# Performance work log

Measured on AMD Instinct MI355X. Metric: run time of the kernel, lower is better.

The kernel has to match this reference:

```python
import jax, jax.numpy as jnp
import numpy as np

B = 4096
D_IN = 1024
HIDDEN = [1024, 512, 256]
NUM_DOMAINS = 8


def _glorot(key, shape):
    fan_in, fan_out = shape[-2], shape[-1]
    std = np.sqrt(2.0 / (fan_in + fan_out)).astype(np.float32)
    return jax.random.normal(key, shape, dtype=jnp.float32) * std


def setup_inputs() -> dict:
    key = jax.random.key(0)
    keys = jax.random.split(key, 16)
    dims = [D_IN] + HIDDEN  # per-layer (in, out) = (dims[i], dims[i+1])
    inp = {
        "x": jax.random.normal(keys[0], (B, D_IN), dtype=jnp.float32),
        "indicator": jax.random.randint(keys[1], (B,), 0, NUM_DOMAINS, dtype=jnp.int32),
    }
    for i in range(len(HIDDEN)):
        inp[f"sk{i}"] = _glorot(keys[2 + i], (dims[i], dims[i + 1]))
        inp[f"sb{i}"] = jnp.zeros((dims[i + 1],), dtype=jnp.float32)
        # per-domain kernels stacked on leading domain axis: (D, in, out)
        inp[f"dk{i}"] = _glorot(keys[6 + i], (NUM_DOMAINS, dims[i], dims[i + 1]))
        inp[f"db{i}"] = jnp.zeros((NUM_DOMAINS, dims[i + 1]), dtype=jnp.float32)
    return inp


def reference(x, indicator, sk0, sb0, dk0, db0, sk1, sb1, dk1, db1, sk2, sb2, dk2, db2):
    shared_k = [sk0, sk1, sk2]
    shared_b = [sb0, sb1, sb2]
    domain_k = [dk0, dk1, dk2]
    domain_b = [db0, db1, db2]
    D = dk0.shape[0]
    # Replicate input across all domains: [B, D, d_in] (source computes every domain stack)
    h = jnp.broadcast_to(x[:, None, :], (x.shape[0], D, x.shape[1]))
    for sk, sb, dk, db in zip(shared_k, shared_b, domain_k, domain_b):
        w_eff = sk[None, :, :] * dk          # [D, in, out]  fused shared*domain weights
        b_eff = sb[None, :] + db             # [D, out]
        h = jnp.einsum('bdi,dio->bdo', h, w_eff) + b_eff[None, :, :]
        h = jax.nn.relu(h)                   # all layers use 'relu' (no output_activation)
    one_hot = jax.nn.one_hot(indicator, D, dtype=h.dtype)  # [B, D]
    return jnp.einsum('bdo,bd->bo', h, one_hot)
```

## Files before the change

### kernel.cpp

```cpp
#include <hip/hip_runtime.h>

#define NROWS 4096
#define NDOM 8

typedef short short8 __attribute__((ext_vector_type(8)));
typedef float floatx4 __attribute__((ext_vector_type(4)));
typedef unsigned short ushort8v __attribute__((ext_vector_type(8)));

__device__ __forceinline__ unsigned short f2bf(float f) {
    union { float f; unsigned u; } v; v.f = f;
    unsigned r = v.u + 0x7FFFu + ((v.u >> 16) & 1u);
    return (unsigned short)(r >> 16);
}

__device__ __forceinline__ void dma16(const void* g, void* l) {
    __builtin_amdgcn_global_load_lds(
        (const __attribute__((address_space(1))) unsigned*)g,
        (__attribute__((address_space(3))) unsigned*)l, 16, 0, 0);
}

template <int N>
__device__ __forceinline__ void wait_vmcnt() {
    static_assert(N == 0 || N == 2 || N == 3 || N == 4 || N == 6 || N == 8, "unsupported vmcnt");
    if constexpr (N == 0) asm volatile("s_waitcnt vmcnt(0)" ::: "memory");
    else if constexpr (N == 2) asm volatile("s_waitcnt vmcnt(2)" ::: "memory");
    else if constexpr (N == 3) asm volatile("s_waitcnt vmcnt(3)" ::: "memory");
    else if constexpr (N == 4) asm volatile("s_waitcnt vmcnt(4)" ::: "memory");
    else if constexpr (N == 6) asm volatile("s_waitcnt vmcnt(6)" ::: "memory");
    else if constexpr (N == 8) asm volatile("s_waitcnt vmcnt(8)" ::: "memory");
}


template <int K, int N>
__device__ __forceinline__ void weff_tile(const float* __restrict__ sk,
                                          const float* __restrict__ dk,
                                          unsigned short* __restrict__ wt,
                                          unsigned short* __restrict__ lds,
                                          int local) {
    const int d = local & 7;
    const int rest = local >> 3;
    const int k0 = (rest & (K / 256 - 1)) * 256;
    const int n0 = (rest / (K / 256)) * 64;
    const int t = threadIdx.x;

    const int n = t & 63;
    const int kg = (t >> 6) * 64;
#pragma unroll
    for (int c8 = 0; c8 < 8; ++c8) {
        const int kb = k0 + kg + c8 * 8;
        unsigned short wb[8];
#pragma unroll
        for (int i = 0; i < 8; ++i) {
            int k = kb + i;
            wb[i] = f2bf(sk[(size_t)k * N + n0 + n] * dk[((size_t)d * K + k) * N + n0 + n]);
        }
        int ch = (kg + c8 * 8) >> 3;
        int phys = ch ^ (n & 31);
        *(ushort8v*)&lds[n * 256 + phys * 8] = *(ushort8v*)wb;
    }
    __syncthreads();

#pragma unroll
    for (int it = 0; it < 4; ++it) {
        const int nn = (t >> 4) + it * 16;
        const int c = t & 15;
        ushort8v a = *(ushort8v*)&lds[nn * 256 + ((2 * c) ^ (nn & 31)) * 8];
        ushort8v b = *(ushort8v*)&lds[nn * 256 + ((2 * c + 1) ^ (nn & 31)) * 8];
        unsigned short* dst = wt + ((size_t)d * N + n0 + nn) * K + k0 + c * 16;
        *(ushort8v*)dst = a;
        *(ushort8v*)(dst + 8) = b;
    }
}

__global__ void precompute_kernel(const float* __restrict__ x,
                                  const int* __restrict__ ind,
                                  const float* __restrict__ sk0, const float* __restrict__ dk0,
                                  const float* __restrict__ sk1, const float* __restrict__ dk1,
                                  const float* __restrict__ sk2, const float* __restrict__ dk2,
                                  unsigned short* __restrict__ xb,
                                  unsigned short* __restrict__ w0t,
                                  unsigned short* __restrict__ w1t,
                                  unsigned short* __restrict__ w2t,
                                  int* __restrict__ offsets,
                                  int* __restrict__ rowidx) {
    __shared__ union SMem {
        unsigned short wtile[64 * 256];
        struct {
            unsigned short cnt[256][NDOM];
            int base[256][NDOM];
            int dom_total[NDOM];
            int dom_off[NDOM + 1];
        } sort;
    } smem;

    const int b = blockIdx.x;
    const int t = threadIdx.x;

    if (b < 256) {
#pragma unroll
        for (int pass = 0; pass < 8; ++pass) {
            int row = b * 16 + pass * 2 + (t >> 7);
            int ch = t & 127;
            const float* src = x + (size_t)row * 1024 + ch * 8;
            floatx4 v0 = *(const floatx4*)src;
            floatx4 v1 = *(const floatx4*)(src + 4);
            unsigned short o[8];
            o[0] = f2bf(v0[0]); o[1] = f2bf(v0[1]); o[2] = f2bf(v0[2]); o[3] = f2bf(v0[3]);
            o[4] = f2bf(v1[0]); o[5] = f2bf(v1[1]); o[6] = f2bf(v1[2]); o[7] = f2bf(v1[3]);
            *(ushort8v*)(xb + (size_t)row * 1024 + ch * 8) = *(ushort8v*)o;
        }
    } else if (b < 256 + 512) {
        weff_tile<1024, 1024>(sk0, dk0, w0t, smem.wtile, b - 256);
    } else if (b < 256 + 512 + 256) {
        weff_tile<1024, 512>(sk1, dk1, w1t, smem.wtile, b - (256 + 512));
    } else if (b < 256 + 512 + 256 + 64) {
        weff_tile<512, 256>(sk2, dk2, w2t, smem.wtile, b - (256 + 512 + 256));
    } else {
        int myind[16];
#pragma unroll
        for (int i = 0; i < 16; ++i) myind[i] = ind[t * 16 + i];
        unsigned short c[NDOM];
#pragma unroll
        for (int d = 0; d < NDOM; ++d) c[d] = 0;
#pragma unroll
        for (int i = 0; i < 16; ++i) c[myind[i]]++;
#pragma unroll
        for (int d = 0; d < NDOM; ++d) smem.sort.cnt[t][d] = c[d];
        __syncthreads();
        if (t < NDOM) {
            int acc = 0;
            for (int ch = 0; ch < 256; ++ch) { smem.sort.base[ch][t] = acc; acc += smem.sort.cnt[ch][t]; }
            smem.sort.dom_total[t] = acc;
        }
        __syncthreads();
        if (t == 0) {
            int acc = 0;
            for (int d = 0; d < NDOM; ++d) { smem.sort.dom_off[d] = acc; acc += smem.sort.dom_total[d]; }
            smem.sort.dom_off[NDOM] = acc;
        }
        __syncthreads();
        int pos[NDOM];
#pragma unroll
        for (int d = 0; d < NDOM; ++d) pos[d] = smem.sort.dom_off[d] + smem.sort.base[t][d];
#pragma unroll
        for (int i = 0; i < 16; ++i) {
            int dm = myind[i];
            rowidx[pos[dm]++] = t * 16 + i;
        }
        if (t <= NDOM) offsets[t] = smem.sort.dom_off[t];
    }
}

template <int FM, int FN, int MSLOTS, int K, int N, bool GATHER, bool SCATTER>
__launch_bounds__(256)
__global__ void star_gemm(const unsigned short* __restrict__ Ab,
                          const unsigned short* __restrict__ Wt,
                          const float* __restrict__ sb,
                          const float* __restrict__ db,
                          float* __restrict__ OutF,
                          unsigned short* __restrict__ OutB,
                          const int* __restrict__ offsets,
                          const int* __restrict__ rowidx) {
    constexpr int BM = 32 * FM;
    constexpr int BN = 32 * FN;
    constexpr int NK = K / 64;
    constexpr int AI = BM / 32;
    constexpr int WI = BN / 32;
    constexpr int CNT = AI + WI;

    __shared__ __align__(128) unsigned short As[2][BM * 64];
    __shared__ __align__(128) unsigned short Ws[2][BN * 64];

    const int gid = blockIdx.x;
    const int d = gid & 7;
    const int mslot = (gid >> 3) % MSLOTS;
    const int n0 = (gid / (8 * MSLOTS)) * BN;

    const int bstart = offsets[d];
    const int bend = offsets[d + 1];
    const int bsize = bend - bstart;

    const int tid = threadIdx.x;
    const int lane = tid & 63;
    const int w = tid >> 6;
    const int wy = w >> 1;
    const int wx = w & 1;
    const int lm = lane & 15;
    const int quad = lane >> 4;

    const int lrow = lane >> 3;
    const int phys = lane & 7;

    float bias[FN];
#pragma unroll
    for (int j = 0; j < FN; ++j) {
        int n = n0 + wx * FN * 16 + j * 16 + lm;
        bias[j] = sb[n] + db[d * N + n];
    }

    const unsigned short* wsrc[WI];
#pragma unroll
    for (int j = 0; j < WI; ++j) {
        int nr0 = (w * WI + j) * 8;
        int nn = nr0 + lrow;
        int ch = phys ^ (nn & 7);
        wsrc[j] = Wt + ((size_t)d * N + n0 + nn) * K + ch * 8;
    }

    for (int mt = mslot; mt * BM < bsize; mt += MSLOTS) {
        const int row_start = bstart + mt * BM;

        const unsigned short* asrc[AI];
#pragma unroll
        for (int j = 0; j < AI; ++j) {
            int m0 = (w * AI + j) * 8;
            int mm = m0 + lrow;
            int ch = phys ^ (mm & 7);
            int p = row_start + mm; if (p >= bend) p = bend - 1;
            int src = GATHER ? rowidx[p] : p;
            asrc[j] = Ab + (size_t)src * K + ch * 8;
        }

        auto dma_tiles = [&](int kt, int buf) {
            const int k0 = kt * 64;
#pragma unroll
            for (int j = 0; j < AI; ++j)
                dma16(asrc[j] + k0, &As[buf][(w * AI + j) * 512]);
#pragma unroll
            for (int j = 0; j < WI; ++j)
                dma16(wsrc[j] + k0, &Ws[buf][(w * WI + j) * 512]);
        };

        dma_tiles(0, 0);

        floatx4 acc[FM][FN];
#pragma unroll
        for (int i = 0; i < FM; ++i)
#pragma unroll
            for (int j = 0; j < FN; ++j) acc[i][j] = floatx4{0.f, 0.f, 0.f, 0.f};

#pragma unroll 2
        for (int kt = 0; kt < NK; ++kt) {
            const int buf = kt & 1;
            if (kt + 1 < NK) {
                dma_tiles(kt + 1, 1 - buf);
                wait_vmcnt<CNT>();
            } else {
                wait_vmcnt<0>();
            }
            __builtin_amdgcn_s_barrier();
            asm volatile("" ::: "memory");

            short8 av[2][FM], wv[2][FN];
#pragma unroll
            for (int kk = 0; kk < 2; ++kk) {
#pragma unroll
                for (int i = 0; i < FM; ++i) {
                    int m = wy * FM * 16 + i * 16 + lm;
                    int pc = (kk * 4 + quad) ^ (m & 7);
                    av[kk][i] = *(const short8*)&As[buf][m * 64 + pc * 8];
                }
#pragma unroll
                for (int j = 0; j < FN; ++j) {
                    int n = wx * FN * 16 + j * 16 + lm;
                    int pc = (kk * 4 + quad) ^ (n & 7);
                    wv[kk][j] = *(const short8*)&Ws[buf][n * 64 + pc * 8];
                }
            }
            asm volatile("s_waitcnt lgkmcnt(0)" ::: "memory");
            __builtin_amdgcn_sched_barrier(0);
            __builtin_amdgcn_s_barrier();
            asm volatile("" ::: "memory");

            __builtin_amdgcn_s_setprio(1);
#pragma unroll
            for (int kk = 0; kk < 2; ++kk)
#pragma unroll
                for (int i = 0; i < FM; ++i)
#pragma unroll
                    for (int j = 0; j < FN; ++j)
                        acc[i][j] = __builtin_amdgcn_mfma_f32_16x16x32_bf16(
                            av[kk][i], wv[kk][j], acc[i][j], 0, 0, 0);
            __builtin_amdgcn_s_setprio(0);
        }

#pragma unroll
        for (int i = 0; i < FM; ++i) {
#pragma unroll
            for (int rg = 0; rg < 4; ++rg) {
                int m = wy * FM * 16 + i * 16 + quad * 4 + rg;
                int p = row_start + m;
                if (p < bend) {
                    if constexpr (SCATTER) {
                        int orow = rowidx[p];
#pragma unroll
                        for (int j = 0; j < FN; ++j) {
                            int n = n0 + wx * FN * 16 + j * 16 + lm;
                            float v = acc[i][j][rg] + bias[j];
                            OutF[(size_t)orow * N + n] = v > 0.f ? v : 0.f;
                        }
                    } else {
#pragma unroll
                        for (int j = 0; j < FN; ++j) {
                            int n = n0 + wx * FN * 16 + j * 16 + lm;
                            float v = acc[i][j][rg] + bias[j];
                            OutB[(size_t)p * N + n] = f2bf(v > 0.f ? v : 0.f);
                        }
                    }
                }
            }
        }
    }
}

extern "C" void kernel_launch(void* const* d_in, const int* in_sizes, int n_in,
                              void* d_out, int out_size, void* d_ws, size_t ws_size,
                              hipStream_t stream) {
    const float* x = (const float*)d_in[0];
    const int* ind = (const int*)d_in[1];
    const float* sk0 = (const float*)d_in[2];
    const float* sb0 = (const float*)d_in[3];
    const float* dk0 = (const float*)d_in[4];
    const float* db0 = (const float*)d_in[5];
    const float* sk1 = (const float*)d_in[6];
    const float* sb1 = (const float*)d_in[7];
    const float* dk1 = (const float*)d_in[8];
    const float* db1 = (const float*)d_in[9];
    const float* sk2 = (const float*)d_in[10];
    const float* sb2 = (const float*)d_in[11];
    const float* dk2 = (const float*)d_in[12];
    const float* db2 = (const float*)d_in[13];
    float* out = (float*)d_out;

    char* ws = (char*)d_ws;
    int* offsets = (int*)ws;
    int* rowidx = (int*)(ws + 256);
    unsigned short* xb  = (unsigned short*)(ws + 32768);
    unsigned short* h1  = xb + (size_t)NROWS * 1024;
    unsigned short* h2  = h1 + (size_t)NROWS * 1024;
    unsigned short* w0t = h2 + (size_t)NROWS * 512;
    unsigned short* w1t = w0t + (size_t)NDOM * 1024 * 1024;
    unsigned short* w2t = w1t + (size_t)NDOM * 512 * 1024;

    precompute_kernel<<<256 + 512 + 256 + 64 + 1, 256, 0, stream>>>(
        x, ind, sk0, dk0, sk1, dk1, sk2, dk2, xb, w0t, w1t, w2t, offsets, rowidx);

    star_gemm<2, 2, 8, 1024, 1024, true, false><<<1024, 256, 0, stream>>>(
        xb, w0t, sb0, db0, nullptr, h1, offsets, rowidx);
    star_gemm<2, 2, 8, 1024, 512, false, false><<<512, 256, 0, stream>>>(
        h1, w1t, sb1, db1, nullptr, h2, offsets, rowidx);
    star_gemm<1, 2, 16, 512, 256, false, true><<<512, 256, 0, stream>>>(
        h2, w2t, sb2, db2, out, nullptr, offsets, rowidx);
}
```

Baseline: 191.2 us.

## Overlap layer-1/2 weight prep with layer-0 GEMM in a fused launch

Moves the fused weight computation for layers 1 and 2 out of the precompute kernel and into extra blocks of the layer-0 GEMM launch, so that weight preparation runs concurrently with the first GEMM instead of before it. The GEMM body is factored into a device function that takes shared-memory pointers, and layer 0 switches to a wider N tile (FN=4) with half as many GEMM blocks. This shortens the critical path of the precompute stage. In exchange the layer-0 GEMM blocks share the GPU with weight-prep blocks, and the wider tile changes occupancy and register use.

New measurement: 192.8 us. About the same (+0.8%).

```diff
diff --git a/kernel.cpp b/kernel.cpp
--- a/kernel.cpp
+++ b/kernel.cpp
@@ -29,7 +29,6 @@
     else if constexpr (N == 6) asm volatile("s_waitcnt vmcnt(6)" ::: "memory");
     else if constexpr (N == 8) asm volatile("s_waitcnt vmcnt(8)" ::: "memory");
 }
-
 
 template <int K, int N>
 __device__ __forceinline__ void weff_tile(const float* __restrict__ sk,
@@ -75,12 +74,8 @@
 __global__ void precompute_kernel(const float* __restrict__ x,
                                   const int* __restrict__ ind,
                                   const float* __restrict__ sk0, const float* __restrict__ dk0,
-                                  const float* __restrict__ sk1, const float* __restrict__ dk1,
-                                  const float* __restrict__ sk2, const float* __restrict__ dk2,
                                   unsigned short* __restrict__ xb,
                                   unsigned short* __restrict__ w0t,
-                                  unsigned short* __restrict__ w1t,
-                                  unsigned short* __restrict__ w2t,
                                   int* __restrict__ offsets,
                                   int* __restrict__ rowidx) {
     __shared__ union SMem {
@@ -111,10 +106,6 @@
         }
     } else if (b < 256 + 512) {
         weff_tile<1024, 1024>(sk0, dk0, w0t, smem.wtile, b - 256);
-    } else if (b < 256 + 512 + 256) {
-        weff_tile<1024, 512>(sk1, dk1, w1t, smem.wtile, b - (256 + 512));
-    } else if (b < 256 + 512 + 256 + 64) {
-        weff_tile<512, 256>(sk2, dk2, w2t, smem.wtile, b - (256 + 512 + 256));
     } else {
         int myind[16];
 #pragma unroll
@@ -148,6 +139,169 @@
             rowidx[pos[dm]++] = t * 16 + i;
         }
         if (t <= NDOM) offsets[t] = smem.sort.dom_off[t];
+    }
+}
+
+template <int FM, int FN, int MSLOTS, int K, int N, bool GATHER, bool SCATTER>
+__device__ __forceinline__ void star_gemm_body(
+        unsigned short* __restrict__ As,
+        unsigned short* __restrict__ Ws,
+        const unsigned short* __restrict__ Ab,
+        const unsigned short* __restrict__ Wt,
+        const float* __restrict__ sb,
+        const float* __restrict__ db,
+        float* __restrict__ OutF,
+        unsigned short* __restrict__ OutB,
+        const int* __restrict__ offsets,
+        const int* __restrict__ rowidx,
+        int gid) {
+    constexpr int BM = 32 * FM;
+    constexpr int BN = 32 * FN;
+    constexpr int NK = K / 64;
+    constexpr int AI = BM / 32;
+    constexpr int WI = BN / 32;
+    constexpr int CNT = AI + WI;
+    constexpr int ASZ = BM * 64;
+    constexpr int WSZ = BN * 64;
+
+    const int d = gid & 7;
+    const int mslot = (gid >> 3) % MSLOTS;
+    const int n0 = (gid / (8 * MSLOTS)) * BN;
+
+    const int bstart = offsets[d];
+    const int bend = offsets[d + 1];
+    const int bsize = bend - bstart;
+
+    const int tid = threadIdx.x;
+    const int lane = tid & 63;
+    const int w = tid >> 6;
+    const int wy = w >> 1;
+    const int wx = w & 1;
+    const int lm = lane & 15;
+    const int quad = lane >> 4;
+
+    const int lrow = lane >> 3;
+    const int phys = lane & 7;
+
+    float bias[FN];
+#pragma unroll
+    for (int j = 0; j < FN; ++j) {
+        int n = n0 + wx * FN * 16 + j * 16 + lm;
+        bias[j] = sb[n] + db[d * N + n];
+    }
+
+    const unsigned short* wsrc[WI];
+#pragma unroll
+    for (int j = 0; j < WI; ++j) {
+        int nr0 = (w * WI + j) * 8;
+        int nn = nr0 + lrow;
+        int ch = phys ^ (nn & 7);
+        wsrc[j] = Wt + ((size_t)d * N + n0 + nn) * K + ch * 8;
+    }
+
+    for (int mt = mslot; mt * BM < bsize; mt += MSLOTS) {
+        const int row_start = bstart + mt * BM;
+
+        const unsigned short* asrc[AI];
+#pragma unroll
+        for (int j = 0; j < AI; ++j) {
+            int m0 = (w * AI + j) * 8;
+            int mm = m0 + lrow;
+            int ch = phys ^ (mm & 7);
+            int p = row_start + mm; if (p >= bend) p = bend - 1;
+            int src = GATHER ? rowidx[p] : p;
+            asrc[j] = Ab + (size_t)src * K + ch * 8;
+        }
+
+        auto dma_tiles = [&](int kt, int buf) {
+            const int k0 = kt * 64;
+#pragma unroll
+            for (int j = 0; j < AI; ++j)
+                dma16(asrc[j] + k0, &As[buf * ASZ + (w * AI + j) * 512]);
+#pragma unroll
+            for (int j = 0; j < WI; ++j)
+                dma16(wsrc[j] + k0, &Ws[buf * WSZ + (w * WI + j) * 512]);
+        };
+
+        dma_tiles(0, 0);
+
+        floatx4 acc[FM][FN];
+#pragma unroll
+        for (int i = 0; i < FM; ++i)
+#pragma unroll
+            for (int j = 0; j < FN; ++j) acc[i][j] = floatx4{0.f, 0.f, 0.f, 0.f};
+
+#pragma unroll 2
+        for (int kt = 0; kt < NK; ++kt) {
+            const int buf = kt & 1;
+            if (kt + 1 < NK) {
+                dma_tiles(kt + 1, 1 - buf);
+                wait_vmcnt<CNT>();
+            } else {
+                wait_vmcnt<0>();
+            }
+            __builtin_amdgcn_s_barrier();
+            asm volatile("" ::: "memory");
+
+            short8 av[2][FM], wv[2][FN];
+#pragma unroll
+            for (int kk = 0; kk < 2; ++kk) {
+#pragma unroll
+                for (int i = 0; i < FM; ++i) {
+                    int m = wy * FM * 16 + i * 16 + lm;
+                    int pc = (kk * 4 + quad) ^ (m & 7);
+                    av[kk][i] = *(const short8*)&As[buf * ASZ + m * 64 + pc * 8];
+                }
+#pragma unroll
+                for (int j = 0; j < FN; ++j) {
+                    int n = wx * FN * 16 + j * 16 + lm;
+                    int pc = (kk * 4 + quad) ^ (n & 7);
+                    wv[kk][j] = *(const short8*)&Ws[buf * WSZ + n * 64 + pc * 8];
+                }
+            }
+            asm volatile("s_waitcnt lgkmcnt(0)" ::: "memory");
+            __builtin_amdgcn_sched_barrier(0);
+            __builtin_amdgcn_s_barrier();
+            asm volatile("" ::: "memory");
+
+            __builtin_amdgcn_s_setprio(1);
+#pragma unroll
+            for (int kk = 0; kk < 2; ++kk)
+#pragma unroll
+                for (int i = 0; i < FM; ++i)
+#pragma unroll
+                    for (int j = 0; j < FN; ++j)
+                        acc[i][j] = __builtin_amdgcn_mfma_f32_16x16x32_bf16(
+                            av[kk][i], wv[kk][j], acc[i][j], 0, 0, 0);
+            __builtin_amdgcn_s_setprio(0);
+        }
+
+#pragma unroll
+        for (int i = 0; i < FM; ++i) {
+#pragma unroll
+            for (int rg = 0; rg < 4; ++rg) {
+                int m = wy * FM * 16 + i * 16 + quad * 4 + rg;
+                int p = row_start + m;
+                if (p < bend) {
+                    if constexpr (SCATTER) {
+                        int orow = rowidx[p];
+#pragma unroll
+                        for (int j = 0; j < FN; ++j) {
+                            int n = n0 + wx * FN * 16 + j * 16 + lm;
+                            float v = acc[i][j][rg] + bias[j];
+                            OutF[(size_t)orow * N + n] = v > 0.f ? v : 0.f;
+                        }
+                    } else {
+#pragma unroll
+                        for (int j = 0; j < FN; ++j) {
+                            int n = n0 + wx * FN * 16 + j * 16 + lm;
+                            float v = acc[i][j][rg] + bias[j];
+                            OutB[(size_t)p * N + n] = f2bf(v > 0.f ? v : 0.f);
+                        }
+                    }
+                }
+            }
+        }
     }
 }
 
@@ -163,153 +317,32 @@
                           const int* __restrict__ rowidx) {
     constexpr int BM = 32 * FM;
     constexpr int BN = 32 * FN;
-    constexpr int NK = K / 64;
-    constexpr int AI = BM / 32;
-    constexpr int WI = BN / 32;
-    constexpr int CNT = AI + WI;
-
-    __shared__ __align__(128) unsigned short As[2][BM * 64];
-    __shared__ __align__(128) unsigned short Ws[2][BN * 64];
-
+    __shared__ __align__(128) unsigned short As[2 * BM * 64];
+    __shared__ __align__(128) unsigned short Ws[2 * BN * 64];
+    star_gemm_body<FM, FN, MSLOTS, K, N, GATHER, SCATTER>(
+        As, Ws, Ab, Wt, sb, db, OutF, OutB, offsets, rowidx, blockIdx.x);
+}
+
+__launch_bounds__(256)
+__global__ void l0_fused(const unsigned short* __restrict__ xb,
+                         const unsigned short* __restrict__ w0t,
+                         const float* __restrict__ sb0, const float* __restrict__ db0,
+                         unsigned short* __restrict__ h1,
+                         const float* __restrict__ sk1, const float* __restrict__ dk1,
+                         unsigned short* __restrict__ w1t,
+                         const float* __restrict__ sk2, const float* __restrict__ dk2,
+                         unsigned short* __restrict__ w2t,
+                         const int* __restrict__ offsets,
+                         const int* __restrict__ rowidx) {
+    __shared__ __align__(128) unsigned short smem[24576];
     const int gid = blockIdx.x;
-    const int d = gid & 7;
-    const int mslot = (gid >> 3) % MSLOTS;
-    const int n0 = (gid / (8 * MSLOTS)) * BN;
-
-    const int bstart = offsets[d];
-    const int bend = offsets[d + 1];
-    const int bsize = bend - bstart;
-
-    const int tid = threadIdx.x;
-    const int lane = tid & 63;
-    const int w = tid >> 6;
-    const int wy = w >> 1;
-    const int wx = w & 1;
-    const int lm = lane & 15;
-    const int quad = lane >> 4;
-
-    const int lrow = lane >> 3;
-    const int phys = lane & 7;
-
-    float bias[FN];
-#pragma unroll
-    for (int j = 0; j < FN; ++j) {
-        int n = n0 + wx * FN * 16 + j * 16 + lm;
-        bias[j] = sb[n] + db[d * N + n];
-    }
-
-    const unsigned short* wsrc[WI];
-#pragma unroll
-    for (int j = 0; j < WI; ++j) {
-        int nr0 = (w * WI + j) * 8;
-        int nn = nr0 + lrow;
-        int ch = phys ^ (nn & 7);
-        wsrc[j] = Wt + ((size_t)d * N + n0 + nn) * K + ch * 8;
-    }
-
-    for (int mt = mslot; mt * BM < bsize; mt += MSLOTS) {
-        const int row_start = bstart + mt * BM;
-
-        const unsigned short* asrc[AI];
-#pragma unroll
-        for (int j = 0; j < AI; ++j) {
-            int m0 = (w * AI + j) * 8;
-            int mm = m0 + lrow;
-            int ch = phys ^ (mm & 7);
-            int p = row_start + mm; if (p >= bend) p = bend - 1;
-            int src = GATHER ? rowidx[p] : p;
-            asrc[j] = Ab + (size_t)src * K + ch * 8;
-        }
-
-        auto dma_tiles = [&](int kt, int buf) {
-            const int k0 = kt * 64;
-#pragma unroll
-            for (int j = 0; j < AI; ++j)
-                dma16(asrc[j] + k0, &As[buf][(w * AI + j) * 512]);
-#pragma unroll
-            for (int j = 0; j < WI; ++j)
-                dma16(wsrc[j] + k0, &Ws[buf][(w * WI + j) * 512]);
-        };
-
-        dma_tiles(0, 0);
-
-        floatx4 acc[FM][FN];
-#pragma unroll
-        for (int i = 0; i < FM; ++i)
-#pragma unroll
-            for (int j = 0; j < FN; ++j) acc[i][j] = floatx4{0.f, 0.f, 0.f, 0.f};
-
-#pragma unroll 2
-        for (int kt = 0; kt < NK; ++kt) {
-            const int buf = kt & 1;
-            if (kt + 1 < NK) {
-                dma_tiles(kt + 1, 1 - buf);
-                wait_vmcnt<CNT>();
-            } else {
-                wait_vmcnt<0>();
-            }
-            __builtin_amdgcn_s_barrier();
-            asm volatile("" ::: "memory");
-
-            short8 av[2][FM], wv[2][FN];
-#pragma unroll
-            for (int kk = 0; kk < 2; ++kk) {
-#pragma unroll
-                for (int i = 0; i < FM; ++i) {
-                    int m = wy * FM * 16 + i * 16 + lm;
-                    int pc = (kk * 4 + quad) ^ (m & 7);
-                    av[kk][i] = *(const short8*)&As[buf][m * 64 + pc * 8];
-                }
-#pragma unroll
-                for (int j = 0; j < FN; ++j) {
-                    int n = wx * FN * 16 + j * 16 + lm;
-                    int pc = (kk * 4 + quad) ^ (n & 7);
-                    wv[kk][j] = *(const short8*)&Ws[buf][n * 64 + pc * 8];
-                }
-            }
-            asm volatile("s_waitcnt lgkmcnt(0)" ::: "memory");
-            __builtin_amdgcn_sched_barrier(0);
-            __builtin_amdgcn_s_barrier();
-            asm volatile("" ::: "memory");
-
-            __builtin_amdgcn_s_setprio(1);
-#pragma unroll
-            for (int kk = 0; kk < 2; ++kk)
-#pragma unroll
-                for (int i = 0; i < FM; ++i)
-#pragma unroll
-                    for (int j = 0; j < FN; ++j)
-                        acc[i][j] = __builtin_amdgcn_mfma_f32_16x16x32_bf16(
-                            av[kk][i], wv[kk][j], acc[i][j], 0, 0, 0);
-            __builtin_amdgcn_s_setprio(0);
-        }
-
-#pragma unroll
-        for (int i = 0; i < FM; ++i) {
-#pragma unroll
-            for (int rg = 0; rg < 4; ++rg) {
-                int m = wy * FM * 16 + i * 16 + quad * 4 + rg;
-                int p = row_start + m;
-                if (p < bend) {
-                    if constexpr (SCATTER) {
-                        int orow = rowidx[p];
-#pragma unroll
-                        for (int j = 0; j < FN; ++j) {
-                            int n = n0 + wx * FN * 16 + j * 16 + lm;
-                            float v = acc[i][j][rg] + bias[j];
-                            OutF[(size_t)orow * N + n] = v > 0.f ? v : 0.f;
-                        }
-                    } else {
-#pragma unroll
-                        for (int j = 0; j < FN; ++j) {
-                            int n = n0 + wx * FN * 16 + j * 16 + lm;
-                            float v = acc[i][j][rg] + bias[j];
-                            OutB[(size_t)p * N + n] = f2bf(v > 0.f ? v : 0.f);
-                        }
-                    }
-                }
-            }
-        }
+    if (gid < 512) {
+        star_gemm_body<2, 4, 8, 1024, 1024, true, false>(
+            smem, smem + 8192, xb, w0t, sb0, db0, nullptr, h1, offsets, rowidx, gid);
+    } else if (gid < 512 + 256) {
+        weff_tile<1024, 512>(sk1, dk1, w1t, smem, gid - 512);
+    } else {
+        weff_tile<512, 256>(sk2, dk2, w2t, smem, gid - (512 + 256));
     }
 }
 
@@ -342,11 +375,12 @@
     unsigned short* w1t = w0t + (size_t)NDOM * 1024 * 1024;
     unsigned short* w2t = w1t + (size_t)NDOM * 512 * 1024;
 
-    precompute_kernel<<<256 + 512 + 256 + 64 + 1, 256, 0, stream>>>(
-        x, ind, sk0, dk0, sk1, dk1, sk2, dk2, xb, w0t, w1t, w2t, offsets, rowidx);
-
-    star_gemm<2, 2, 8, 1024, 1024, true, false><<<1024, 256, 0, stream>>>(
-        xb, w0t, sb0, db0, nullptr, h1, offsets, rowidx);
+    precompute_kernel<<<256 + 512 + 1, 256, 0, stream>>>(
+        x, ind, sk0, dk0, xb, w0t, offsets, rowidx);
+
+    l0_fused<<<512 + 256 + 64, 256, 0, stream>>>(
+        xb, w0t, sb0, db0, h1, sk1, dk1, w1t, sk2, dk2, w2t, offsets, rowidx);
+
     star_gemm<2, 2, 8, 1024, 512, false, false><<<512, 256, 0, stream>>>(
         h1, w1t, sb1, db1, nullptr, h2, offsets, rowidx);
     star_gemm<1, 2, 16, 512, 256, false, true><<<512, 256, 0, stream>>>(
```

## Fuse precompute and three GEMM layers into one cooperative persistent kernel

Applied to the files above, without the earlier changes.

Replaces four separate launches with a single cooperative kernel of 256 blocks × 512 threads that loops over precompute work items and then runs each GEMM layer, separated by grid-wide syncs. GEMM tiles are reshaped for 8 waves (2×4) with larger BN, and MSLOTS for layer 0 drops to 4, which changes the per-block work distribution. It aims to remove launch gaps and tail effects between stages, at the cost of grid.sync overhead and only one 512-thread block per CU, which limits occupancy and latency hiding.

After: 470.5 us. +146.1%, slower.

```diff
diff --git a/kernel.cpp b/kernel.cpp
--- a/kernel.cpp
+++ b/kernel.cpp
@@ -1,4 +1,7 @@
 #include <hip/hip_runtime.h>
+#include <hip/hip_cooperative_groups.h>
+
+namespace cg = cooperative_groups;
 
 #define NROWS 4096
 #define NDOM 8
@@ -21,15 +24,12 @@
 
 template <int N>
 __device__ __forceinline__ void wait_vmcnt() {
-    static_assert(N == 0 || N == 2 || N == 3 || N == 4 || N == 6 || N == 8, "unsupported vmcnt");
+    static_assert(N == 0 || N == 2 || N == 3 || N == 4, "unsupported vmcnt");
     if constexpr (N == 0) asm volatile("s_waitcnt vmcnt(0)" ::: "memory");
     else if constexpr (N == 2) asm volatile("s_waitcnt vmcnt(2)" ::: "memory");
     else if constexpr (N == 3) asm volatile("s_waitcnt vmcnt(3)" ::: "memory");
     else if constexpr (N == 4) asm volatile("s_waitcnt vmcnt(4)" ::: "memory");
-    else if constexpr (N == 6) asm volatile("s_waitcnt vmcnt(6)" ::: "memory");
-    else if constexpr (N == 8) asm volatile("s_waitcnt vmcnt(8)" ::: "memory");
-}
-
+}
 
 template <int K, int N>
 __device__ __forceinline__ void weff_tile(const float* __restrict__ sk,
@@ -44,9 +44,9 @@
     const int t = threadIdx.x;
 
     const int n = t & 63;
-    const int kg = (t >> 6) * 64;
-#pragma unroll
-    for (int c8 = 0; c8 < 8; ++c8) {
+    const int kg = (t >> 6) * 32;
+#pragma unroll
+    for (int c8 = 0; c8 < 4; ++c8) {
         const int kb = k0 + kg + c8 * 8;
         unsigned short wb[8];
 #pragma unroll
@@ -61,8 +61,8 @@
     __syncthreads();
 
 #pragma unroll
-    for (int it = 0; it < 4; ++it) {
-        const int nn = (t >> 4) + it * 16;
+    for (int it = 0; it < 2; ++it) {
+        const int nn = (t >> 4) + it * 32;
         const int c = t & 15;
         ushort8v a = *(ushort8v*)&lds[nn * 256 + ((2 * c) ^ (nn & 31)) * 8];
         ushort8v b = *(ushort8v*)&lds[nn * 256 + ((2 * c + 1) ^ (nn & 31)) * 8];
@@ -72,51 +72,37 @@
     }
 }
 
-__global__ void precompute_kernel(const float* __restrict__ x,
-                                  const int* __restrict__ ind,
-                                  const float* __restrict__ sk0, const float* __restrict__ dk0,
-                                  const float* __restrict__ sk1, const float* __restrict__ dk1,
-                                  const float* __restrict__ sk2, const float* __restrict__ dk2,
-                                  unsigned short* __restrict__ xb,
-                                  unsigned short* __restrict__ w0t,
-                                  unsigned short* __restrict__ w1t,
-                                  unsigned short* __restrict__ w2t,
-                                  int* __restrict__ offsets,
-                                  int* __restrict__ rowidx) {
-    __shared__ union SMem {
-        unsigned short wtile[64 * 256];
-        struct {
-            unsigned short cnt[256][NDOM];
-            int base[256][NDOM];
-            int dom_total[NDOM];
-            int dom_off[NDOM + 1];
-        } sort;
-    } smem;
-
-    const int b = blockIdx.x;
+__device__ __forceinline__ void xb_task(const float* __restrict__ x,
+                                        unsigned short* __restrict__ xb, int b) {
     const int t = threadIdx.x;
-
-    if (b < 256) {
-#pragma unroll
-        for (int pass = 0; pass < 8; ++pass) {
-            int row = b * 16 + pass * 2 + (t >> 7);
-            int ch = t & 127;
-            const float* src = x + (size_t)row * 1024 + ch * 8;
-            floatx4 v0 = *(const floatx4*)src;
-            floatx4 v1 = *(const floatx4*)(src + 4);
-            unsigned short o[8];
-            o[0] = f2bf(v0[0]); o[1] = f2bf(v0[1]); o[2] = f2bf(v0[2]); o[3] = f2bf(v0[3]);
-            o[4] = f2bf(v1[0]); o[5] = f2bf(v1[1]); o[6] = f2bf(v1[2]); o[7] = f2bf(v1[3]);
-            *(ushort8v*)(xb + (size_t)row * 1024 + ch * 8) = *(ushort8v*)o;
-        }
-    } else if (b < 256 + 512) {
-        weff_tile<1024, 1024>(sk0, dk0, w0t, smem.wtile, b - 256);
-    } else if (b < 256 + 512 + 256) {
-        weff_tile<1024, 512>(sk1, dk1, w1t, smem.wtile, b - (256 + 512));
-    } else if (b < 256 + 512 + 256 + 64) {
-        weff_tile<512, 256>(sk2, dk2, w2t, smem.wtile, b - (256 + 512 + 256));
-    } else {
-        int myind[16];
+#pragma unroll
+    for (int pass = 0; pass < 4; ++pass) {
+        int row = b * 16 + pass * 4 + (t >> 7);
+        int ch = t & 127;
+        const float* src = x + (size_t)row * 1024 + ch * 8;
+        floatx4 v0 = *(const floatx4*)src;
+        floatx4 v1 = *(const floatx4*)(src + 4);
+        unsigned short o[8];
+        o[0] = f2bf(v0[0]); o[1] = f2bf(v0[1]); o[2] = f2bf(v0[2]); o[3] = f2bf(v0[3]);
+        o[4] = f2bf(v1[0]); o[5] = f2bf(v1[1]); o[6] = f2bf(v1[2]); o[7] = f2bf(v1[3]);
+        *(ushort8v*)(xb + (size_t)row * 1024 + ch * 8) = *(ushort8v*)o;
+    }
+}
+
+struct SortMem {
+    unsigned short cnt[256][NDOM];
+    int base[256][NDOM];
+    int dom_total[NDOM];
+    int dom_off[NDOM + 1];
+};
+
+__device__ __forceinline__ void sort_task(const int* __restrict__ ind,
+                                          int* __restrict__ offsets,
+                                          int* __restrict__ rowidx,
+                                          SortMem& s) {
+    const int t = threadIdx.x;
+    int myind[16];
+    if (t < 256) {
 #pragma unroll
         for (int i = 0; i < 16; ++i) myind[i] = ind[t * 16 + i];
         unsigned short c[NDOM];
@@ -125,53 +111,61 @@
 #pragma unroll
         for (int i = 0; i < 16; ++i) c[myind[i]]++;
 #pragma unroll
-        for (int d = 0; d < NDOM; ++d) smem.sort.cnt[t][d] = c[d];
-        __syncthreads();
-        if (t < NDOM) {
-            int acc = 0;
-            for (int ch = 0; ch < 256; ++ch) { smem.sort.base[ch][t] = acc; acc += smem.sort.cnt[ch][t]; }
-            smem.sort.dom_total[t] = acc;
-        }
-        __syncthreads();
-        if (t == 0) {
-            int acc = 0;
-            for (int d = 0; d < NDOM; ++d) { smem.sort.dom_off[d] = acc; acc += smem.sort.dom_total[d]; }
-            smem.sort.dom_off[NDOM] = acc;
-        }
-        __syncthreads();
+        for (int d = 0; d < NDOM; ++d) s.cnt[t][d] = c[d];
+    }
+    __syncthreads();
+    if (t < NDOM) {
+        int acc = 0;
+        for (int ch = 0; ch < 256; ++ch) { s.base[ch][t] = acc; acc += s.cnt[ch][t]; }
+        s.dom_total[t] = acc;
+    }
+    __syncthreads();
+    if (t == 0) {
+        int acc = 0;
+        for (int d = 0; d < NDOM; ++d) { s.dom_off[d] = acc; acc += s.dom_total[d]; }
+        s.dom_off[NDOM] = acc;
+    }
+    __syncthreads();
+    if (t < 256) {
         int pos[NDOM];
 #pragma unroll
-        for (int d = 0; d < NDOM; ++d) pos[d] = smem.sort.dom_off[d] + smem.sort.base[t][d];
+        for (int d = 0; d < NDOM; ++d) pos[d] = s.dom_off[d] + s.base[t][d];
 #pragma unroll
         for (int i = 0; i < 16; ++i) {
             int dm = myind[i];
             rowidx[pos[dm]++] = t * 16 + i;
         }
-        if (t <= NDOM) offsets[t] = smem.sort.dom_off[t];
+        if (t <= NDOM) offsets[t] = s.dom_off[t];
     }
 }
 
 template <int FM, int FN, int MSLOTS, int K, int N, bool GATHER, bool SCATTER>
-__launch_bounds__(256)
-__global__ void star_gemm(const unsigned short* __restrict__ Ab,
-                          const unsigned short* __restrict__ Wt,
-                          const float* __restrict__ sb,
-                          const float* __restrict__ db,
-                          float* __restrict__ OutF,
-                          unsigned short* __restrict__ OutB,
-                          const int* __restrict__ offsets,
-                          const int* __restrict__ rowidx) {
-    constexpr int BM = 32 * FM;
-    constexpr int BN = 32 * FN;
+__device__ __forceinline__ void star_gemm_body(
+        unsigned short* __restrict__ As,
+        unsigned short* __restrict__ Ws,
+        const unsigned short* __restrict__ Ab,
+        const unsigned short* __restrict__ Wt,
+        const float* __restrict__ sb,
+        const float* __restrict__ db,
+        float* __restrict__ OutF,
+        unsigned short* __restrict__ OutB,
+        const int* __restrict__ offsets,
+        const int* __restrict__ rowidx,
+        int gid) {
+    constexpr int WM = 2, WN = 4, NW = 8;
+    constexpr int BM = WM * FM * 16;
+    constexpr int BN = WN * FN * 16;
     constexpr int NK = K / 64;
-    constexpr int AI = BM / 32;
-    constexpr int WI = BN / 32;
-    constexpr int CNT = AI + WI;
-
-    __shared__ __align__(128) unsigned short As[2][BM * 64];
-    __shared__ __align__(128) unsigned short Ws[2][BN * 64];
-
-    const int gid = blockIdx.x;
+    constexpr int AI_TOT = BM / 8;
+    constexpr int WI_TOT = BN / 8;
+    constexpr int A_PER = AI_TOT / NW, A_REM = AI_TOT % NW;
+    constexpr int W_PER = WI_TOT / NW;
+    static_assert(WI_TOT % NW == 0, "W dma must be wave-uniform");
+    constexpr int AI_MAX = (AI_TOT + NW - 1) / NW;
+    constexpr int CNT = A_PER + W_PER;
+    constexpr int ASZ = BM * 64;
+    constexpr int WSZ = BN * 64;
+
     const int d = gid & 7;
     const int mslot = (gid >> 3) % MSLOTS;
     const int n0 = (gid / (8 * MSLOTS)) * BN;
@@ -183,8 +177,8 @@
     const int tid = threadIdx.x;
     const int lane = tid & 63;
     const int w = tid >> 6;
-    const int wy = w >> 1;
-    const int wx = w & 1;
+    const int wy = w >> 2;
+    const int wx = w & 3;
     const int lm = lane & 15;
     const int quad = lane >> 4;
 
@@ -198,37 +192,43 @@
         bias[j] = sb[n] + db[d * N + n];
     }
 
-    const unsigned short* wsrc[WI];
-#pragma unroll
-    for (int j = 0; j < WI; ++j) {
-        int nr0 = (w * WI + j) * 8;
-        int nn = nr0 + lrow;
+    const unsigned short* wsrc[W_PER];
+#pragma unroll
+    for (int jj = 0; jj < W_PER; ++jj) {
+        int j = w + jj * NW;
+        int nn = j * 8 + lrow;
         int ch = phys ^ (nn & 7);
-        wsrc[j] = Wt + ((size_t)d * N + n0 + nn) * K + ch * 8;
+        wsrc[jj] = Wt + ((size_t)d * N + n0 + nn) * K + ch * 8;
     }
 
     for (int mt = mslot; mt * BM < bsize; mt += MSLOTS) {
         const int row_start = bstart + mt * BM;
 
-        const unsigned short* asrc[AI];
-#pragma unroll
-        for (int j = 0; j < AI; ++j) {
-            int m0 = (w * AI + j) * 8;
-            int mm = m0 + lrow;
-            int ch = phys ^ (mm & 7);
-            int p = row_start + mm; if (p >= bend) p = bend - 1;
-            int src = GATHER ? rowidx[p] : p;
-            asrc[j] = Ab + (size_t)src * K + ch * 8;
+        const unsigned short* asrc[AI_MAX];
+#pragma unroll
+        for (int jj = 0; jj < AI_MAX; ++jj) {
+            int j = w + jj * NW;
+            if (j < AI_TOT) {
+                int mm = j * 8 + lrow;
+                int ch = phys ^ (mm & 7);
+                int p = row_start + mm; if (p >= bend) p = bend - 1;
+                int src = GATHER ? rowidx[p] : p;
+                asrc[jj] = Ab + (size_t)src * K + ch * 8;
+            }
         }
 
         auto dma_tiles = [&](int kt, int buf) {
             const int k0 = kt * 64;
 #pragma unroll
-            for (int j = 0; j < AI; ++j)
-                dma16(asrc[j] + k0, &As[buf][(w * AI + j) * 512]);
-#pragma unroll
-            for (int j = 0; j < WI; ++j)
-                dma16(wsrc[j] + k0, &Ws[buf][(w * WI + j) * 512]);
+            for (int jj = 0; jj < AI_MAX; ++jj) {
+                int j = w + jj * NW;
+                if (j < AI_TOT) dma16(asrc[jj] + k0, &As[buf * ASZ + j * 512]);
+            }
+#pragma unroll
+            for (int jj = 0; jj < W_PER; ++jj) {
+                int j = w + jj * NW;
+                dma16(wsrc[jj] + k0, &Ws[buf * WSZ + j * 512]);
+            }
         };
 
         dma_tiles(0, 0);
@@ -244,7 +244,11 @@
             const int buf = kt & 1;
             if (kt + 1 < NK) {
                 dma_tiles(kt + 1, 1 - buf);
-                wait_vmcnt<CNT>();
+                if constexpr (A_REM == 0) {
+                    wait_vmcnt<CNT>();
+                } else {
+                    if (w < A_REM) wait_vmcnt<CNT + 1>(); else wait_vmcnt<CNT>();
+                }
             } else {
                 wait_vmcnt<0>();
             }
@@ -258,13 +262,13 @@
                 for (int i = 0; i < FM; ++i) {
                     int m = wy * FM * 16 + i * 16 + lm;
                     int pc = (kk * 4 + quad) ^ (m & 7);
-                    av[kk][i] = *(const short8*)&As[buf][m * 64 + pc * 8];
+                    av[kk][i] = *(const short8*)&As[buf * ASZ + m * 64 + pc * 8];
                 }
 #pragma unroll
                 for (int j = 0; j < FN; ++j) {
                     int n = wx * FN * 16 + j * 16 + lm;
                     int pc = (kk * 4 + quad) ^ (n & 7);
-                    wv[kk][j] = *(const short8*)&Ws[buf][n * 64 + pc * 8];
+                    wv[kk][j] = *(const short8*)&Ws[buf * WSZ + n * 64 + pc * 8];
                 }
             }
             asm volatile("s_waitcnt lgkmcnt(0)" ::: "memory");
@@ -311,6 +315,67 @@
             }
         }
     }
+}
+
+union SMemAll {
+    unsigned short gemm[24576];
+    unsigned short wtile[64 * 256];
+    SortMem sort;
+};
+
+__launch_bounds__(512, 1)
+__global__ void star_all(const float* __restrict__ x,
+                         const int* __restrict__ ind,
+                         const float* __restrict__ sk0, const float* __restrict__ dk0,
+                         const float* __restrict__ sk1, const float* __restrict__ dk1,
+                         const float* __restrict__ sk2, const float* __restrict__ dk2,
+                         const float* __restrict__ sb0, const float* __restrict__ db0,
+                         const float* __restrict__ sb1, const float* __restrict__ db1,
+                         const float* __restrict__ sb2, const float* __restrict__ db2,
+                         float* __restrict__ out,
+                         unsigned short* __restrict__ xb,
+                         unsigned short* __restrict__ h1,
+                         unsigned short* __restrict__ h2,
+                         unsigned short* __restrict__ w0t,
+                         unsigned short* __restrict__ w1t,
+                         unsigned short* __restrict__ w2t,
+                         int* __restrict__ offsets,
+                         int* __restrict__ rowidx) {
+    __shared__ __align__(128) SMemAll smem;
+    cg::grid_group grid = cg::this_grid();
+
+    for (int item = blockIdx.x; item < 1089; item += 256) {
+        if (item < 256) {
+            xb_task(x, xb, item);
+        } else if (item < 768) {
+            weff_tile<1024, 1024>(sk0, dk0, w0t, smem.wtile, item - 256);
+        } else if (item == 768) {
+            sort_task(ind, offsets, rowidx, smem.sort);
+        } else if (item < 1025) {
+            weff_tile<1024, 512>(sk1, dk1, w1t, smem.wtile, item - 769);
+        } else {
+            weff_tile<512, 256>(sk2, dk2, w2t, smem.wtile, item - 1025);
+        }
+        __syncthreads();
+    }
+    __threadfence();
+    grid.sync();
+
+    star_gemm_body<2, 2, 4, 1024, 1024, true, false>(
+        smem.gemm, smem.gemm + 8192, xb, w0t, sb0, db0, nullptr, h1,
+        offsets, rowidx, blockIdx.x);
+    __threadfence();
+    grid.sync();
+
+    star_gemm_body<2, 2, 8, 1024, 512, false, false>(
+        smem.gemm, smem.gemm + 8192, h1, w1t, sb1, db1, nullptr, h2,
+        offsets, rowidx, blockIdx.x);
+    __threadfence();
+    grid.sync();
+
+    star_gemm_body<1, 2, 16, 512, 256, false, true>(
+        smem.gemm, smem.gemm + 4096, h2, w2t, sb2, db2, out, nullptr,
+        offsets, rowidx, blockIdx.x);
 }
 
 extern "C" void kernel_launch(void* const* d_in, const int* in_sizes, int n_in,
@@ -342,13 +407,15 @@
     unsigned short* w1t = w0t + (size_t)NDOM * 1024 * 1024;
     unsigned short* w2t = w1t + (size_t)NDOM * 512 * 1024;
 
-    precompute_kernel<<<256 + 512 + 256 + 64 + 1, 256, 0, stream>>>(
-        x, ind, sk0, dk0, sk1, dk1, sk2, dk2, xb, w0t, w1t, w2t, offsets, rowidx);
-
-    star_gemm<2, 2, 8, 1024, 1024, true, false><<<1024, 256, 0, stream>>>(
-        xb, w0t, sb0, db0, nullptr, h1, offsets, rowidx);
-    star_gemm<2, 2, 8, 1024, 512, false, false><<<512, 256, 0, stream>>>(
-        h1, w1t, sb1, db1, nullptr, h2, offsets, rowidx);
-    star_gemm<1, 2, 16, 512, 256, false, true><<<512, 256, 0, stream>>>(
-        h2, w2t, sb2, db2, out, nullptr, offsets, rowidx);
-}
+    void* args[] = {
+        (void*)&x, (void*)&ind,
+        (void*)&sk0, (void*)&dk0, (void*)&sk1, (void*)&dk1, (void*)&sk2, (void*)&dk2,
+        (void*)&sb0, (void*)&db0, (void*)&sb1, (void*)&db1, (void*)&sb2, (void*)&db2,
+        (void*)&out,
+        (void*)&xb, (void*)&h1, (void*)&h2,
+        (void*)&w0t, (void*)&w1t, (void*)&w2t,
+        (void*)&offsets, (void*)&rowidx
+    };
+    hipLaunchCooperativeKernel((void*)star_all, dim3(256), dim3(512),
+                               args, 0, stream);
+}
```

## Pre-tile fused weights into MFMA-ready blocks and drop LDS transpose in precompute

Applied to the files above, without the earlier changes.

The precompute stage now writes the fused bf16 weights (shared times domain) straight into a blocked layout of 16-column by K chunks that match the GEMM's LDS tile shape. It does this from registers with vectorized float4 loads, so the LDS transpose and the barrier are gone and fewer, larger blocks do the work. The GEMM's weight DMA addresses and LDS fragment reads are changed to match the new layout and no longer use the XOR swizzle. This targets the cost of the weight-precompute pass and its shared-memory round trip. The unswizzled LDS reads may cause bank conflicts, and each thread now holds more registers.

New measurement: 209.3 us. 1.09x slower.

```diff
diff --git a/kernel.cpp b/kernel.cpp
--- a/kernel.cpp
+++ b/kernel.cpp
@@ -30,47 +30,51 @@
     else if constexpr (N == 8) asm volatile("s_waitcnt vmcnt(8)" ::: "memory");
 }
 
-
 template <int K, int N>
-__device__ __forceinline__ void weff_tile(const float* __restrict__ sk,
-                                          const float* __restrict__ dk,
-                                          unsigned short* __restrict__ wt,
-                                          unsigned short* __restrict__ lds,
-                                          int local) {
+__device__ __forceinline__ void weff_tile_nolds(const float* __restrict__ sk,
+                                                const float* __restrict__ dk,
+                                                unsigned short* __restrict__ wt,
+                                                int local) {
+    constexpr int KT = K / 512;
     const int d = local & 7;
     const int rest = local >> 3;
-    const int k0 = (rest & (K / 256 - 1)) * 256;
-    const int n0 = (rest / (K / 256)) * 64;
+    const int kt = rest & (KT - 1);
+    const int nt = rest / KT;
+    const int k0 = kt * 512;
+    const int n0 = nt * 64;
     const int t = threadIdx.x;
-
-    const int n = t & 63;
-    const int kg = (t >> 6) * 64;
-#pragma unroll
-    for (int c8 = 0; c8 < 8; ++c8) {
-        const int kb = k0 + kg + c8 * 8;
-        unsigned short wb[8];
-#pragma unroll
-        for (int i = 0; i < 8; ++i) {
-            int k = kb + i;
-            wb[i] = f2bf(sk[(size_t)k * N + n0 + n] * dk[((size_t)d * K + k) * N + n0 + n]);
-        }
-        int ch = (kg + c8 * 8) >> 3;
-        int phys = ch ^ (n & 31);
-        *(ushort8v*)&lds[n * 256 + phys * 8] = *(ushort8v*)wb;
-    }
-    __syncthreads();
-
-#pragma unroll
-    for (int it = 0; it < 4; ++it) {
-        const int nn = (t >> 4) + it * 16;
-        const int c = t & 15;
-        ushort8v a = *(ushort8v*)&lds[nn * 256 + ((2 * c) ^ (nn & 31)) * 8];
-        ushort8v b = *(ushort8v*)&lds[nn * 256 + ((2 * c + 1) ^ (nn & 31)) * 8];
-        unsigned short* dst = wt + ((size_t)d * N + n0 + nn) * K + k0 + c * 16;
-        *(ushort8v*)dst = a;
-        *(ushort8v*)(dst + 8) = b;
-    }
-}
+    const int ng = t & 3;
+    const int kg = t >> 2;
+    const int kb = k0 + kg * 8;
+    const int nb = n0 + ng * 16;
+
+    unsigned short ob[16][8];
+#pragma unroll
+    for (int i = 0; i < 8; ++i) {
+        const int k = kb + i;
+        const float* srow = sk + (size_t)k * N + nb;
+        const float* drow = dk + ((size_t)d * K + k) * N + nb;
+#pragma unroll
+        for (int q = 0; q < 4; ++q) {
+            floatx4 sv = *(const floatx4*)(srow + q * 4);
+            floatx4 dv = *(const floatx4*)(drow + q * 4);
+#pragma unroll
+            for (int j = 0; j < 4; ++j) ob[q * 4 + j][i] = f2bf(sv[j] * dv[j]);
+        }
+    }
+    unsigned short* dst = wt + ((size_t)d * (N / 16) + (nb >> 4)) * ((size_t)K * 16)
+                             + (size_t)(kb >> 3) * 128;
+#pragma unroll
+    for (int nn = 0; nn < 16; ++nn)
+        *(ushort8v*)(dst + nn * 8) = *(ushort8v*)ob[nn];
+}
+
+struct SortMem {
+    unsigned short cnt[256][NDOM];
+    int base[256][NDOM];
+    int dom_total[NDOM];
+    int dom_off[NDOM + 1];
+};
 
 __global__ void precompute_kernel(const float* __restrict__ x,
                                   const int* __restrict__ ind,
@@ -83,23 +87,22 @@
                                   unsigned short* __restrict__ w2t,
                                   int* __restrict__ offsets,
                                   int* __restrict__ rowidx) {
-    __shared__ union SMem {
-        unsigned short wtile[64 * 256];
-        struct {
-            unsigned short cnt[256][NDOM];
-            int base[256][NDOM];
-            int dom_total[NDOM];
-            int dom_off[NDOM + 1];
-        } sort;
-    } smem;
+    __shared__ SortMem smem;
 
     const int b = blockIdx.x;
     const int t = threadIdx.x;
 
     if (b < 256) {
+        weff_tile_nolds<1024, 1024>(sk0, dk0, w0t, b);
+    } else if (b < 256 + 128) {
+        weff_tile_nolds<1024, 512>(sk1, dk1, w1t, b - 256);
+    } else if (b < 256 + 128 + 32) {
+        weff_tile_nolds<512, 256>(sk2, dk2, w2t, b - (256 + 128));
+    } else if (b < 256 + 128 + 32 + 256) {
+        const int bb = b - (256 + 128 + 32);
 #pragma unroll
         for (int pass = 0; pass < 8; ++pass) {
-            int row = b * 16 + pass * 2 + (t >> 7);
+            int row = bb * 16 + pass * 2 + (t >> 7);
             int ch = t & 127;
             const float* src = x + (size_t)row * 1024 + ch * 8;
             floatx4 v0 = *(const floatx4*)src;
@@ -109,12 +112,6 @@
             o[4] = f2bf(v1[0]); o[5] = f2bf(v1[1]); o[6] = f2bf(v1[2]); o[7] = f2bf(v1[3]);
             *(ushort8v*)(xb + (size_t)row * 1024 + ch * 8) = *(ushort8v*)o;
         }
-    } else if (b < 256 + 512) {
-        weff_tile<1024, 1024>(sk0, dk0, w0t, smem.wtile, b - 256);
-    } else if (b < 256 + 512 + 256) {
-        weff_tile<1024, 512>(sk1, dk1, w1t, smem.wtile, b - (256 + 512));
-    } else if (b < 256 + 512 + 256 + 64) {
-        weff_tile<512, 256>(sk2, dk2, w2t, smem.wtile, b - (256 + 512 + 256));
     } else {
         int myind[16];
 #pragma unroll
@@ -125,29 +122,29 @@
 #pragma unroll
         for (int i = 0; i < 16; ++i) c[myind[i]]++;
 #pragma unroll
-        for (int d = 0; d < NDOM; ++d) smem.sort.cnt[t][d] = c[d];
+        for (int d = 0; d < NDOM; ++d) smem.cnt[t][d] = c[d];
         __syncthreads();
         if (t < NDOM) {
             int acc = 0;
-            for (int ch = 0; ch < 256; ++ch) { smem.sort.base[ch][t] = acc; acc += smem.sort.cnt[ch][t]; }
-            smem.sort.dom_total[t] = acc;
+            for (int ch = 0; ch < 256; ++ch) { smem.base[ch][t] = acc; acc += smem.cnt[ch][t]; }
+            smem.dom_total[t] = acc;
         }
         __syncthreads();
         if (t == 0) {
             int acc = 0;
-            for (int d = 0; d < NDOM; ++d) { smem.sort.dom_off[d] = acc; acc += smem.sort.dom_total[d]; }
-            smem.sort.dom_off[NDOM] = acc;
+            for (int d = 0; d < NDOM; ++d) { smem.dom_off[d] = acc; acc += smem.dom_total[d]; }
+            smem.dom_off[NDOM] = acc;
         }
         __syncthreads();
         int pos[NDOM];
 #pragma unroll
-        for (int d = 0; d < NDOM; ++d) pos[d] = smem.sort.dom_off[d] + smem.sort.base[t][d];
+        for (int d = 0; d < NDOM; ++d) pos[d] = smem.dom_off[d] + smem.base[t][d];
 #pragma unroll
         for (int i = 0; i < 16; ++i) {
             int dm = myind[i];
             rowidx[pos[dm]++] = t * 16 + i;
         }
-        if (t <= NDOM) offsets[t] = smem.sort.dom_off[t];
+        if (t <= NDOM) offsets[t] = smem.dom_off[t];
     }
 }
 
@@ -201,10 +198,9 @@
     const unsigned short* wsrc[WI];
 #pragma unroll
     for (int j = 0; j < WI; ++j) {
-        int nr0 = (w * WI + j) * 8;
-        int nn = nr0 + lrow;
-        int ch = phys ^ (nn & 7);
-        wsrc[j] = Wt + ((size_t)d * N + n0 + nn) * K + ch * 8;
+        int u = w * WI + j;
+        wsrc[j] = Wt + ((size_t)d * (N / 16) + (n0 >> 4) + (u >> 1)) * ((size_t)K * 16)
+                     + (u & 1) * 512 + lane * 8;
     }
 
     for (int mt = mslot; mt * BM < bsize; mt += MSLOTS) {
@@ -228,7 +224,7 @@
                 dma16(asrc[j] + k0, &As[buf][(w * AI + j) * 512]);
 #pragma unroll
             for (int j = 0; j < WI; ++j)
-                dma16(wsrc[j] + k0, &Ws[buf][(w * WI + j) * 512]);
+                dma16(wsrc[j] + kt * 1024, &Ws[buf][(w * WI + j) * 512]);
         };
 
         dma_tiles(0, 0);
@@ -262,9 +258,9 @@
                 }
 #pragma unroll
                 for (int j = 0; j < FN; ++j) {
-                    int n = wx * FN * 16 + j * 16 + lm;
-                    int pc = (kk * 4 + quad) ^ (n & 7);
-                    wv[kk][j] = *(const short8*)&Ws[buf][n * 64 + pc * 8];
+                    int goff = (wx * FN + j) * 1024;
+                    int c = kk * 4 + quad;
+                    wv[kk][j] = *(const short8*)&Ws[buf][goff + c * 128 + lm * 8];
                 }
             }
             asm volatile("s_waitcnt lgkmcnt(0)" ::: "memory");
@@ -342,7 +338,7 @@
     unsigned short* w1t = w0t + (size_t)NDOM * 1024 * 1024;
     unsigned short* w2t = w1t + (size_t)NDOM * 512 * 1024;
 
-    precompute_kernel<<<256 + 512 + 256 + 64 + 1, 256, 0, stream>>>(
+    precompute_kernel<<<256 + 128 + 32 + 256 + 1, 256, 0, stream>>>(
         x, ind, sk0, dk0, sk1, dk1, sk2, dk2, xb, w0t, w1t, w2t, offsets, rowidx);
 
     star_gemm<2, 2, 8, 1024, 1024, true, false><<<1024, 256, 0, stream>>>(
```
